# Performance work log

Measured on AMD Instinct MI355X. Metric: run time of the kernel, lower is better.

## Reference

```python
import jax, jax.numpy as jnp
import numpy as np

B, T, D, H, KH = 4, 2048, 2048, 32, 64  # batch, seq, n_dim(=n_dim_att), heads, head_size
DMIX, DDEC, NMIX = 32, 64, 5
N_LAYER, LAYER_ID = 24, 0


def setup_inputs() -> dict:
    key = jax.random.key(0)
    ks = jax.random.split(key, 16)
    rn = lambda k, s, scale: jax.random.normal(k, s, jnp.float32) * scale
    un = lambda k, s: jax.random.uniform(k, s, jnp.float32, -0.01, 0.01)

    # init-formula parameters (layer_id=0 -> ratio_0_to_1=0, ratio_1_to_almost0=1)
    ddd = np.arange(D, dtype=np.float32) / D
    tmx = (1.0 - ddd)[None, None, :]
    tmr = (1.0 - ddd ** 0.5)[None, None, :]
    n = np.arange(D, dtype=np.float32)
    decay_speed = (-6.0 + 5.0 * (n / (D - 1)) ** 0.7)[None, None, :]

    inp = {
        'x': rn(ks[0], (B, T, D), 1.0),
        'shift_state_in': rn(ks[1], (B, D), 1.0),
        'wkv_state_in': rn(ks[2], (B, H, KH, KH), 0.1),
        'time_maa_x': jnp.asarray(tmx),
        'time_maa_r': jnp.asarray(tmr),
        'time_maa_k': jnp.asarray(tmx),
        'time_maa_v': jnp.asarray(tmx),
        'time_maa_w': jnp.asarray(tmx),
        'time_maa_v2': jnp.asarray(tmx),
        'time_maa_w1': un(ks[3], (D, NMIX * DMIX)),
        'time_maa_w2': un(ks[4], (NMIX, DMIX, D)),
        'time_decay': jnp.asarray(decay_speed),
        'time_decay_w1': un(ks[5], (D, DDEC)),
        'time_decay_w2': un(ks[6], (DDEC, D)),
        'time_value2_w1': un(ks[7], (D, DDEC)),
        'time_value2_w2': un(ks[8], (DDEC, D)),
        'W_r': rn(ks[9], (D, D), 0.02),
        'W_k': rn(ks[10], (D, D), 0.02),
        'W_v': rn(ks[11], (D, D), 0.02),
        'W_o': rn(ks[12], (D, D), 0.02),
        'ln_w': jnp.ones((D,), jnp.float32),
        'ln_b': jnp.zeros((D,), jnp.float32),
    }
    return inp


def reference(x, shift_state_in, wkv_state_in,
              time_maa_x, time_maa_r, time_maa_k, time_maa_v, time_maa_w, time_maa_v2,
              time_maa_w1, time_maa_w2, time_decay, time_decay_w1, time_decay_w2,
              time_value2_w1, time_value2_w2, W_r, W_k, W_v, W_o, ln_w, ln_b):
    b, t, d = x.shape
    h, kh = wkv_state_in.shape[1], wkv_state_in.shape[2]

    shift_state_out = x[:, -1]
    xprev = jnp.concatenate([shift_state_in[:, None, :], x[:, :-1]], axis=1)
    dxprev = xprev - x  # [b,t,d]

    # low-rank token-shift mixing: tanh(x @ w1) -> 5 mixing deltas
    xxx = x + dxprev * time_maa_x
    mix = jnp.tanh(xxx @ time_maa_w1).reshape(b, t, NMIX, -1)
    mix = jnp.einsum('btfm,fmd->fbtd', mix, time_maa_w2)  # [5,b,t,d]
    mr, mk, mv, mw, mv2 = mix[0], mix[1], mix[2], mix[3], mix[4]

    xr = x + dxprev * (time_maa_r + mr)
    xk = x + dxprev * (time_maa_k + mk)
    xv = x + dxprev * (time_maa_v + mv)
    xw = x + dxprev * (time_maa_w + mw)
    xv2 = x + dxprev * (time_maa_v2 + mv2)

    r = xr @ W_r
    k = xk @ W_k
    v = xv @ W_v
    # note: v2 uses the SAME value projection plus a low-rank tanh branch
    v2 = xv2 @ W_v + jnp.tanh(xv2 @ time_value2_w1) @ time_value2_w2

    w = time_decay + jnp.tanh(xw @ time_decay_w1) @ time_decay_w2
    decay = jnp.exp(-jnp.exp(w))  # per-channel decay in (0,1)
    k = k * (1.0 - decay)

    # WKV linear-attention recurrence (u = 0): y_t = r_t . S_{t-1};  S_t = decay_t*S_{t-1} + k_t v_t^T
    to_heads = lambda a: a.reshape(b, t, h, kh).transpose(1, 0, 2, 3)  # [t,b,h,kh]
    rt, kt, vt, dt = to_heads(r), to_heads(k), to_heads(v), to_heads(decay)

    def step(S, inp):
        r_, k_, v_, d_ = inp  # each [b,h,kh]
        y = jnp.einsum('bhk,bhkv->bhv', r_, S)
        S = S * d_[..., None] + k_[..., None] * v_[:, :, None, :]
        return S, y

    wkv_state_out, ys = jax.lax.scan(step, wkv_state_in, (rt, kt, vt, dt))
    y = ys.transpose(1, 0, 2, 3).reshape(b, t, d) + v2

    # LayerNorm (ln_x)
    mu = y.mean(-1, keepdims=True)
    var = ((y - mu) ** 2).mean(-1, keepdims=True)
    y = (y - mu) / jnp.sqrt(var + 1e-5) * ln_w + ln_b

    out = y @ W_o
    return out, shift_state_out, wkv_state_out
```

## Files before the change

kernel.cpp:

```cpp
#include <hip/hip_runtime.h>
#include <hip/hip_bf16.h>

typedef __attribute__((ext_vector_type(8))) short   vshort8;
typedef __attribute__((ext_vector_type(8))) unsigned short vushort8;
typedef __attribute__((ext_vector_type(4))) float   vfloat4;
typedef __attribute__((ext_vector_type(2))) float   vfloat2;

__device__ __forceinline__ float bf2f(unsigned short h) {
    union { unsigned u; float f; } x; x.u = ((unsigned)h) << 16; return x.f;
}
__device__ __forceinline__ unsigned short f2bf(float f) {
    union { float f; unsigned u; } x; x.f = f;
    unsigned r = x.u + 0x7fffu + ((x.u >> 16) & 1u);
    return (unsigned short)(r >> 16);
}
__device__ __forceinline__ void cp16_async(const void* g, void* l) {
    __builtin_amdgcn_global_load_lds(
        (const __attribute__((address_space(1))) unsigned int*)g,
        (__attribute__((address_space(3))) unsigned int*)l, 16, 0, 0);
}

#define FBAR() do { asm volatile("" ::: "memory"); __builtin_amdgcn_s_barrier(); asm volatile("" ::: "memory"); } while (0)

#define Bc 4
#define Tc 2048
#define Dc 2048
#define Hc 32
#define KHc 64
#define BTc (Bc*Tc)
#define BTDc ((size_t)BTc*Dc)
#define LP 72

struct EpiP {
    float* of;
    unsigned short* ob;
    const float* a0;
    const float* a1;
    const unsigned short* ab;
    const float* vec;
};

template<int EPI>
__device__ __forceinline__ void epi_store(float a, int row, int col, int N, const EpiP& ep)
{
    size_t o = (size_t)row * N + col;
    if (EPI == 0) {
        ep.of[o] = a;
    } else if (EPI == 1) {
        ep.ob[o] = f2bf(a);
    } else if (EPI == 2) {
        ep.ob[o] = f2bf(tanhf(a));
    } else if (EPI == 4) {
        ep.ob[o] = f2bf(a * (1.f - ep.a0[o]));
    } else if (EPI == 5) {
        ep.of[o] = expf(-expf(ep.vec[col] + a));
    } else if (EPI == 6) {
        ep.ob[o] = f2bf(a + bf2f(ep.ab[o]));
    }
}

template<int EPI>
__global__ __launch_bounds__(256) void gemm_bt(
    const unsigned short* __restrict__ A, int lda,
    const unsigned short* __restrict__ BT, int ldbt,
    int M, int N, int K, EpiP ep)
{
    __shared__ unsigned short lA[128 * 32];
    __shared__ unsigned short lB[128 * 32];
    const int tid  = threadIdx.x;
    const int lane = tid & 63;
    const int w    = tid >> 6;
    const int mt   = blockIdx.y, nt = blockIdx.x;
    const int wm = (w >> 1) * 64, wn = (w & 1) * 64;
    const int frow = lane & 15, fk = (lane >> 4) * 8;

    vfloat4 acc[4][4];
#pragma unroll
    for (int i = 0; i < 4; i++)
#pragma unroll
        for (int j = 0; j < 4; j++) acc[i][j] = vfloat4{0.f, 0.f, 0.f, 0.f};

    for (int k0 = 0; k0 < K; k0 += 32) {
        __syncthreads();
#pragma unroll
        for (int p = 0; p < 2; p++) {
            int idx = p * 256 + tid;
            int row = idx >> 2, colh = (idx & 3) * 8;
            cp16_async(A + (size_t)(mt * 128 + row) * lda + k0 + colh, &lA[idx * 8]);
        }
#pragma unroll
        for (int p = 0; p < 2; p++) {
            int idx = p * 256 + tid;
            int row = idx >> 2, colh = (idx & 3) * 8;
            cp16_async(BT + (size_t)(nt * 128 + row) * ldbt + k0 + colh, &lB[idx * 8]);
        }
        __syncthreads();

        vshort8 af[4], bfr[4];
#pragma unroll
        for (int m = 0; m < 4; m++) af[m]  = *(const vshort8*)&lA[(wm + m * 16 + frow) * 32 + fk];
#pragma unroll
        for (int n = 0; n < 4; n++) bfr[n] = *(const vshort8*)&lB[(wn + n * 16 + frow) * 32 + fk];
#pragma unroll
        for (int m = 0; m < 4; m++)
#pragma unroll
            for (int n = 0; n < 4; n++)
                acc[m][n] = __builtin_amdgcn_mfma_f32_16x16x32_bf16(af[m], bfr[n], acc[m][n], 0, 0, 0);
    }

    const int crow0 = mt * 128 + wm, ccol0 = nt * 128 + wn;
#pragma unroll
    for (int m = 0; m < 4; m++)
#pragma unroll
        for (int n = 0; n < 4; n++) {
            int col = ccol0 + n * 16 + (lane & 15);
            if (col >= N) continue;
#pragma unroll
            for (int q = 0; q < 4; q++) {
                int row = crow0 + m * 16 + (lane >> 4) * 4 + q;
                epi_store<EPI>(acc[m][n][q], row, col, N, ep);
            }
        }
}

template<int EPI>
__global__ __launch_bounds__(512, 1) void gemm256s(
    const unsigned short* __restrict__ A, int lda,
    const unsigned short* __restrict__ BT, int ldbt,
    int M, int N, int K, EpiP ep)
{
    __shared__ unsigned short sh[3 * 16384];
    const int tid  = threadIdx.x;
    const int lane = tid & 63;
    const int w    = tid >> 6;

    int bid = blockIdx.y * gridDim.x + blockIdx.x;
    {
        int nwg = gridDim.x * gridDim.y;
        if ((nwg & 7) == 0) bid = (bid & 7) * (nwg >> 3) + (bid >> 3);
    }
    const int mt = bid / gridDim.x, nt = bid % gridDim.x;

    const int wm = (w >> 2) * 128, wn = (w & 3) * 64;
    const int frow = lane & 15;
    const int cswz = ((lane >> 4) ^ ((frow >> 1) & 3)) * 8;
    const int arow0 = mt * 256, brow0 = nt * 256;

    vfloat4 acc[8][4];
#pragma unroll
    for (int i = 0; i < 8; i++)
#pragma unroll
        for (int j = 0; j < 4; j++) acc[i][j] = vfloat4{0.f, 0.f, 0.f, 0.f};

    const int NT = K >> 5;

    auto stage = [&](int kt, int sbuf) {
        int k0 = kt << 5;
        unsigned short* dst = &sh[sbuf * 16384];
#pragma unroll
        for (int i = 0; i < 2; i++) {
            int idx = i * 512 + tid;
            int row = idx >> 2;
            int ch  = (idx & 3) ^ ((row >> 1) & 3);
            cp16_async(A + (size_t)(arow0 + row) * lda + k0 + ch * 8, dst + idx * 8);
        }
#pragma unroll
        for (int i = 0; i < 2; i++) {
            int idx = i * 512 + tid;
            int row = idx >> 2;
            int ch  = (idx & 3) ^ ((row >> 1) & 3);
            cp16_async(BT + (size_t)(brow0 + row) * ldbt + k0 + ch * 8, dst + 8192 + idx * 8);
        }
    };

    stage(0, 0);
    if (NT > 1) {
        stage(1, 1);
        asm volatile("s_waitcnt vmcnt(4)" ::: "memory");
    } else {
        asm volatile("s_waitcnt vmcnt(0)" ::: "memory");
    }
    __builtin_amdgcn_s_barrier();

    int buf = 0, sb = 2;
    for (int kt = 0; kt < NT; kt++) {
        if (kt + 2 < NT) stage(kt + 2, sb);
        const unsigned short* Ab = &sh[buf * 16384];
        const unsigned short* Bb = Ab + 8192;

        vshort8 af[8], bfv[4];
#pragma unroll
        for (int m = 0; m < 8; m++)
            af[m] = *(const vshort8*)&Ab[(wm + m * 16 + frow) * 32 + cswz];
#pragma unroll
        for (int n = 0; n < 4; n++)
            bfv[n] = *(const vshort8*)&Bb[(wn + n * 16 + frow) * 32 + cswz];

        __builtin_amdgcn_s_setprio(1);
#pragma unroll
        for (int m = 0; m < 8; m++)
#pragma unroll
            for (int n = 0; n < 4; n++)
                acc[m][n] = __builtin_amdgcn_mfma_f32_16x16x32_bf16(af[m], bfv[n], acc[m][n], 0, 0, 0);
        __builtin_amdgcn_s_setprio(0);

        if (kt + 1 < NT) {
            if (kt + 2 < NT) asm volatile("s_waitcnt vmcnt(4)" ::: "memory");
            else             asm volatile("s_waitcnt vmcnt(0)" ::: "memory");
            asm volatile("s_waitcnt lgkmcnt(0)" ::: "memory");
            __builtin_amdgcn_s_barrier();
        }
        buf = (buf == 2) ? 0 : buf + 1;
        sb  = (sb  == 2) ? 0 : sb  + 1;
    }

    const int crow0 = arow0 + wm, ccol0 = brow0 + wn;
#pragma unroll
    for (int m = 0; m < 8; m++)
#pragma unroll
        for (int n = 0; n < 4; n++) {
            int col = ccol0 + n * 16 + (lane & 15);
#pragma unroll
            for (int q = 0; q < 4; q++) {
                int row = crow0 + m * 16 + (lane >> 4) * 4 + q;
                epi_store<EPI>(acc[m][n][q], row, col, N, ep);
            }
        }
}

template<int EPI>
__global__ __launch_bounds__(512, 1) void gemm256p8(
    const unsigned short* __restrict__ A, int lda,
    const unsigned short* __restrict__ BT, int ldbt,
    int M, int N, int K, EpiP ep)
{
    __shared__ unsigned short sh[65536];
    const int tid  = threadIdx.x;
    const int lane = tid & 63;
    const int w    = tid >> 6;

    int bid = blockIdx.y * gridDim.x + blockIdx.x;
    {
        int nwg = gridDim.x * gridDim.y;
        if ((nwg & 7) == 0) bid = (bid & 7) * (nwg >> 3) + (bid >> 3);
    }
    const int mt = bid / gridDim.x, nt = bid % gridDim.x;

    const int wm = (w >> 2) * 128, wn = (w & 3) * 64;
    const int frow = lane & 15;
    const int g    = lane >> 4;
    const int arow0 = mt * 256, brow0 = nt * 256;

    vfloat4 acc[8][4];
#pragma unroll
    for (int i = 0; i < 8; i++)
#pragma unroll
        for (int j = 0; j < 4; j++) acc[i][j] = vfloat4{0.f, 0.f, 0.f, 0.f};

    const int NT = K >> 6;

    auto stageA = [&](int kt, int p) {
        int k0 = kt << 6;
        unsigned short* dst = &sh[(kt & 1) * 32768];
#pragma unroll
        for (int l = 0; l < 2; l++) {
            int idx  = l * 512 + tid;
            int rl   = idx >> 3, slot = idx & 7;
            int rg   = (rl & 63) + p * 64 + ((rl >> 6) << 7);
            int ch   = slot ^ (rg & 7);
            cp16_async(A + (size_t)(arow0 + rg) * lda + k0 + ch * 8, dst + rg * 64 + slot * 8);
        }
    };
    auto stageB = [&](int kt, int p) {
        int k0 = kt << 6;
        unsigned short* dst = &sh[(kt & 1) * 32768 + 16384];
#pragma unroll
        for (int l = 0; l < 2; l++) {
            int idx  = l * 512 + tid;
            int rl   = idx >> 3, slot = idx & 7;
            int rg   = (rl & 31) + p * 32 + ((rl >> 5) << 6);
            int ch   = slot ^ (rg & 7);
            cp16_async(BT + (size_t)(brow0 + rg) * ldbt + k0 + ch * 8, dst + rg * 64 + slot * 8);
        }
    };

    vshort8 af[4][2], bf0[2][2], bf1[2][2];

    auto readA = [&](const unsigned short* Ab, int mh) {
#pragma unroll
        for (int mi = 0; mi < 4; mi++) {
            int r = wm + mh * 64 + mi * 16 + frow;
#pragma unroll
            for (int kk = 0; kk < 2; kk++)
                af[mi][kk] = *(const vshort8*)&Ab[r * 64 + (((kk * 4 + g) ^ (r & 7)) * 8)];
        }
    };
    auto readB = [&](const unsigned short* Bb, int nh, vshort8 (&bfr)[2][2]) {
#pragma unroll
        for (int ni = 0; ni < 2; ni++) {
            int r = wn + nh * 32 + ni * 16 + frow;
#pragma unroll
            for (int kk = 0; kk < 2; kk++)
                bfr[ni][kk] = *(const vshort8*)&Bb[r * 64 + (((kk * 4 + g) ^ (r & 7)) * 8)];
        }
    };
    auto domfma = [&](int mh, int nh, vshort8 (&bfr)[2][2]) {
        __builtin_amdgcn_s_setprio(1);
#pragma unroll
        for (int mi = 0; mi < 4; mi++)
#pragma unroll
            for (int ni = 0; ni < 2; ni++)
#pragma unroll
                for (int kk = 0; kk < 2; kk++)
                    acc[mh * 4 + mi][nh * 2 + ni] = __builtin_amdgcn_mfma_f32_16x16x32_bf16(
                        af[mi][kk], bfr[ni][kk], acc[mh * 4 + mi][nh * 2 + ni], 0, 0, 0);
        __builtin_amdgcn_s_setprio(0);
    };

    stageA(0, 0); stageB(0, 1); stageA(0, 1); stageB(0, 0);
    stageA(1, 0); stageB(1, 1);
    asm volatile("s_waitcnt vmcnt(4)" ::: "memory");
    __builtin_amdgcn_s_barrier();

    const unsigned short* A0 = sh;
    const unsigned short* B0 = sh + 16384;
    const unsigned short* A1 = sh + 32768;
    const unsigned short* B1 = sh + 49152;

    for (int i2 = 0; i2 < NT; i2 += 2) {
        const bool s2 = (i2 + 2 < NT);
        readA(A0, 0); readB(B0, 0, bf0);
        stageA(i2 + 1, 1);
        FBAR();
        asm volatile("s_waitcnt lgkmcnt(0)" ::: "memory");
        domfma(0, 0, bf0);
        FBAR();
        readB(B0, 1, bf1);
        stageB(i2 + 1, 0);
        FBAR();
        asm volatile("s_waitcnt lgkmcnt(0)" ::: "memory");
        domfma(0, 1, bf1);
        FBAR();
        readA(A0, 1);
        if (s2) stageA(i2 + 2, 0);
        FBAR();
        asm volatile("s_waitcnt lgkmcnt(0)" ::: "memory");
        domfma(1, 1, bf1);
        FBAR();
        if (s2) {
            stageB(i2 + 2, 1);
            asm volatile("s_waitcnt vmcnt(4)" ::: "memory");
        } else {
            asm volatile("s_waitcnt vmcnt(0)" ::: "memory");
        }
        FBAR();
        domfma(1, 0, bf0);
        FBAR();
        readA(A1, 0); readB(B1, 0, bf0);
        if (s2) stageA(i2 + 2, 1);
        FBAR();
        asm volatile("s_waitcnt lgkmcnt(0)" ::: "memory");
        domfma(0, 0, bf0);
        FBAR();
        readB(B1, 1, bf1);
        if (s2) stageB(i2 + 2, 0);
        FBAR();
        asm volatile("s_waitcnt lgkmcnt(0)" ::: "memory");
        domfma(0, 1, bf1);
        FBAR();
        readA(A1, 1);
        if (s2) stageA(i2 + 3, 0);
        FBAR();
        asm volatile("s_waitcnt lgkmcnt(0)" ::: "memory");
        domfma(1, 1, bf1);
        FBAR();
        if (s2) {
            stageB(i2 + 3, 1);
            asm volatile("s_waitcnt vmcnt(4)" ::: "memory");
        }
        FBAR();
        domfma(1, 0, bf0);
        FBAR();
    }

    const int crow0 = arow0 + wm, ccol0 = brow0 + wn;
#pragma unroll
    for (int m = 0; m < 8; m++)
#pragma unroll
        for (int n = 0; n < 4; n++) {
            int col = ccol0 + n * 16 + (lane & 15);
#pragma unroll
            for (int q = 0; q < 4; q++) {
                int row = crow0 + m * 16 + (lane >> 4) * 4 + q;
                epi_store<EPI>(acc[m][n][q], row, col, N, ep);
            }
        }
}

struct Mix5P {
    const float* vec[5];
    unsigned short* out[5];
};

__global__ __launch_bounds__(256) void mix5(
    const unsigned short* __restrict__ MP,
    const unsigned short* __restrict__ W2T,
    const float* __restrict__ x,
    const unsigned short* __restrict__ DXb,
    Mix5P p)
{
    __shared__ unsigned short lA[64 * 32];
    __shared__ unsigned short lB[128 * 32];
    const int tid = threadIdx.x, lane = tid & 63, w = tid >> 6;
    const int mt = blockIdx.y, nt = blockIdx.x;
    const int wm = (w >> 1) * 32, wn = (w & 1) * 64;
    const int frow = lane & 15, fk = (lane >> 4) * 8;
    const int row0 = mt * 64, col0 = nt * 128;

    float xr[8][4], dxr[8][4];
#pragma unroll
    for (int mi = 0; mi < 2; mi++)
#pragma unroll
        for (int q = 0; q < 4; q++) {
            int rl = wm + mi * 16 + (lane >> 4) * 4 + q;
            size_t rb = (size_t)(row0 + rl) * Dc + col0;
#pragma unroll
            for (int ni = 0; ni < 4; ni++) {
                int cl = wn + ni * 16 + (lane & 15);
                xr[mi * 4 + q][ni]  = x[rb + cl];
                dxr[mi * 4 + q][ni] = bf2f(DXb[rb + cl]);
            }
        }

    for (int f = 0; f < 5; f++) {
        __syncthreads();
        {
            int row = tid >> 2, ch = tid & 3;
            cp16_async(MP + (size_t)(row0 + row) * 160 + f * 32 + ch * 8, &lA[(row * 4 + ch) * 8]);
        }
#pragma unroll
        for (int p2 = 0; p2 < 2; p2++) {
            int idx = p2 * 256 + tid;
            int row = idx >> 2, ch = idx & 3;
            cp16_async(W2T + (size_t)(col0 + row) * 160 + f * 32 + ch * 8, &lB[(row * 4 + ch) * 8]);
        }
        __syncthreads();

        vshort8 af[2], bfr[4];
#pragma unroll
        for (int mi = 0; mi < 2; mi++) af[mi]  = *(const vshort8*)&lA[(wm + mi * 16 + frow) * 32 + fk];
#pragma unroll
        for (int ni = 0; ni < 4; ni++) bfr[ni] = *(const vshort8*)&lB[(wn + ni * 16 + frow) * 32 + fk];

        vfloat4 acc[2][4];
#pragma unroll
        for (int mi = 0; mi < 2; mi++)
#pragma unroll
            for (int ni = 0; ni < 4; ni++) {
                acc[mi][ni] = vfloat4{0.f, 0.f, 0.f, 0.f};
                acc[mi][ni] = __builtin_amdgcn_mfma_f32_16x16x32_bf16(af[mi], bfr[ni], acc[mi][ni], 0, 0, 0);
            }

        const float* vec = p.vec[f];
        unsigned short* ob = p.out[f];
        float vc[4];
#pragma unroll
        for (int ni = 0; ni < 4; ni++) vc[ni] = vec[col0 + wn + ni * 16 + (lane & 15)];
#pragma unroll
        for (int mi = 0; mi < 2; mi++)
#pragma unroll
            for (int q = 0; q < 4; q++) {
                int rl = wm + mi * 16 + (lane >> 4) * 4 + q;
                size_t rb = (size_t)(row0 + rl) * Dc + col0;
#pragma unroll
                for (int ni = 0; ni < 4; ni++) {
                    int cl = wn + ni * 16 + (lane & 15);
                    ob[rb + cl] = f2bf(xr[mi * 4 + q][ni] + dxr[mi * 4 + q][ni] * (vc[ni] + acc[mi][ni][q]));
                }
            }
    }
}

__global__ __launch_bounds__(256) void prep_xxx(
    const float* __restrict__ x, const float* __restrict__ shift_in,
    const float* __restrict__ tmx, unsigned short* __restrict__ xxx,
    unsigned short* __restrict__ dxb)
{
    int row = blockIdx.x, tid = threadIdx.x;
    int t = row & (Tc - 1), b = row >> 11;
    size_t base = (size_t)row * Dc + tid * 8;
    const float* xp = t ? x + base - Dc : shift_in + (size_t)b * Dc + tid * 8;
    vushort8 o, dxo;
#pragma unroll
    for (int j = 0; j < 8; j++) {
        float xv = x[base + j];
        float dx = xp[j] - xv;
        o[j]   = f2bf(xv + dx * tmx[tid * 8 + j]);
        dxo[j] = f2bf(dx);
    }
    *(vushort8*)(xxx + base) = o;
    *(vushort8*)(dxb + base) = dxo;
}

__global__ __launch_bounds__(256) void shift_copy(const float* __restrict__ x, float* __restrict__ out)
{
    int i = blockIdx.x * 256 + threadIdx.x;
    int b = i >> 11, d = i & (Dc - 1);
    out[i] = x[((size_t)b * Tc + (Tc - 1)) * Dc + d];
}

__global__ __launch_bounds__(256) void transpose_cast(
    const float* __restrict__ in, unsigned short* __restrict__ out, int R, int C)
{
    __shared__ float tile[32][33];
    int ct = blockIdx.x, rt = blockIdx.y;
    int lx = threadIdx.x & 31, ly = threadIdx.x >> 5;
#pragma unroll
    for (int i = 0; i < 4; i++)
        tile[ly + i * 8][lx] = in[(size_t)(rt * 32 + ly + i * 8) * C + ct * 32 + lx];
    __syncthreads();
#pragma unroll
    for (int i = 0; i < 4; i++)
        out[(size_t)(ct * 32 + ly + i * 8) * R + rt * 32 + lx] = f2bf(tile[lx][ly + i * 8]);
}

__global__ __launch_bounds__(256) void wkv_summary(
    const unsigned short* __restrict__ kd, const unsigned short* __restrict__ vv,
    const float* __restrict__ dec, float* __restrict__ P, float* __restrict__ aL)
{
    __shared__ unsigned short kb2T[64][LP];
    __shared__ unsigned short vT[64][LP];
    __shared__ float gp[4][64];
    const int blk = blockIdx.x;
    const int c = blk & 31, bh = blk >> 5, b = bh >> 5, h = bh & 31;
    const int tid = threadIdx.x;
    const size_t rowbase = ((size_t)(b * Tc + c * 64)) * Dc + h * 64;

    {
        int t = tid >> 2, q = tid & 3;
        const unsigned short* src = vv + rowbase + (size_t)t * Dc + q * 16;
        vushort8 a = *(const vushort8*)src;
        vushort8 b2 = *(const vushort8*)(src + 8);
#pragma unroll
        for (int j = 0; j < 8; j++) vT[q * 16 + j][t] = a[j];
#pragma unroll
        for (int j = 0; j < 8; j++) vT[q * 16 + 8 + j][t] = b2[j];
    }

    const int k = tid & 63, grp = tid >> 6;
    const float* decp = dec + rowbase + k;
    const unsigned short* kp = kd + rowbase + k;
    float suf_local[16];
    float pgrp = 1.f;
#pragma unroll
    for (int i = 15; i >= 0; i--) {
        int t = grp * 16 + i;
        float d = decp[(size_t)t * Dc];
        suf_local[i] = pgrp;
        pgrp *= d;
    }
    gp[grp][k] = pgrp;
    __syncthreads();
    float suff = 1.f;
#pragma unroll
    for (int g2 = 0; g2 < 4; g2++) if (g2 > grp) suff *= gp[g2][k];
    if (grp == 0) aL[(size_t)blk * 64 + k] = pgrp * suff;
    {
        vushort8 p0, p1;
#pragma unroll
        for (int i = 0; i < 8; i++) {
            int t = grp * 16 + i;
            p0[i] = f2bf(bf2f(kp[(size_t)t * Dc]) * (suf_local[i] * suff));
        }
#pragma unroll
        for (int i = 0; i < 8; i++) {
            int t = grp * 16 + 8 + i;
            p1[i] = f2bf(bf2f(kp[(size_t)t * Dc]) * (suf_local[8 + i] * suff));
        }
        *(vushort8*)&kb2T[k][grp * 16] = p0;
        *(vushort8*)&kb2T[k][grp * 16 + 8] = p1;
    }
    __syncthreads();

    const int lane = tid & 63, w = tid >> 6;
    const int wm = (w >> 1) * 32, wn = (w & 1) * 32;
    const int frow = lane & 15, fk = (lane >> 4) * 8;
    vfloat4 acc[2][2];
#pragma unroll
    for (int m = 0; m < 2; m++)
#pragma unroll
        for (int n = 0; n < 2; n++) acc[m][n] = vfloat4{0.f, 0.f, 0.f, 0.f};
#pragma unroll
    for (int kk = 0; kk < 2; kk++) {
        vshort8 af[2], bfr[2];
#pragma unroll
        for (int m = 0; m < 2; m++) af[m]  = *(const vshort8*)&kb2T[wm + m * 16 + frow][kk * 32 + fk];
#pragma unroll
        for (int n = 0; n < 2; n++) bfr[n] = *(const vshort8*)&vT[wn + n * 16 + frow][kk * 32 + fk];
#pragma unroll
        for (int m = 0; m < 2; m++)
#pragma unroll
            for (int n = 0; n < 2; n++)
                acc[m][n] = __builtin_amdgcn_mfma_f32_16x16x32_bf16(af[m], bfr[n], acc[m][n], 0, 0, 0);
    }
    float* Pp = P + (size_t)blk * 4096;
#pragma unroll
    for (int m = 0; m < 2; m++)
#pragma unroll
        for (int n = 0; n < 2; n++) {
            int col = wn + n * 16 + (lane & 15);
#pragma unroll
            for (int q = 0; q < 4; q++) {
                int row = wm + m * 16 + (lane >> 4) * 4 + q;
                Pp[row * 64 + col] = acc[m][n][q];
            }
        }
}

__global__ __launch_bounds__(256) void wkv_states(
    const float* __restrict__ wkv_in, float* __restrict__ P ,
    const float* __restrict__ aL, float* __restrict__ wkv_out)
{
    int idx = blockIdx.x * 256 + threadIdx.x;
    int bh = idx >> 12, kv = idx & 4095, k = kv >> 6;
    float S = wkv_in[idx];
    for (int c = 0; c < 32; c++) {
        size_t off = (size_t)bh * 32 + c;
        float p = P[off * 4096 + kv];
        float a = aL[off * 64 + k];
        P[off * 4096 + kv] = S;
        S = S * a + p;
    }
    wkv_out[idx] = S;
}

__global__ __launch_bounds__(256) void wkv_y(
    const unsigned short* __restrict__ rr, const unsigned short* __restrict__ kd,
    const unsigned short* __restrict__ vv, const float* __restrict__ dec,
    const float* __restrict__ Sb, unsigned short* __restrict__ ya)
{
    __shared__ unsigned short rA[64][LP];
    __shared__ unsigned short kbL[64][LP];
    __shared__ unsigned short vT[64][LP];
    __shared__ unsigned short SbT[64][LP];
    __shared__ unsigned short QiM[64][LP];
    __shared__ float gp[4][64];
    const int blk = blockIdx.x;
    const int c = blk & 31, bh = blk >> 5, b = bh >> 5, h = bh & 31;
    const int tid = threadIdx.x;
    const size_t rowbase = ((size_t)(b * Tc + c * 64)) * Dc + h * 64;

    {
        int t = tid >> 2, q = tid & 3;
        const unsigned short* src = vv + rowbase + (size_t)t * Dc + q * 16;
        vushort8 a = *(const vushort8*)src;
        vushort8 b2 = *(const vushort8*)(src + 8);
#pragma unroll
        for (int j = 0; j < 8; j++) vT[q * 16 + j][t] = a[j];
#pragma unroll
        for (int j = 0; j < 8; j++) vT[q * 16 + 8 + j][t] = b2[j];
        const float* sp = Sb + (size_t)blk * 4096 + t * 64 + q * 16;
#pragma unroll
        for (int j = 0; j < 16; j++) SbT[q * 16 + j][t] = f2bf(sp[j]);
    }

    const int k = tid & 63, grp = tid >> 6;
    const float* decp = dec + rowbase + k;
    const unsigned short* rp = rr + rowbase + k;
    const unsigned short* kp = kd + rowbase + k;
    float pref_local[16];
    float pgrp = 1.f;
#pragma unroll
    for (int i = 0; i < 16; i++) {
        int t = grp * 16 + i;
        float d = decp[(size_t)t * Dc];
        pref_local[i] = pgrp;
        pgrp *= d;
    }
    gp[grp][k] = pgrp;
    __syncthreads();
    float pref = 1.f;
#pragma unroll
    for (int g2 = 0; g2 < 4; g2++) if (g2 < grp) pref *= gp[g2][k];
#pragma unroll
    for (int i = 0; i < 16; i++) {
        int t = grp * 16 + i;
        float Aex  = pref * pref_local[i];
        float Ainc = pref * (i < 15 ? pref_local[i + 1] : pgrp);
        rA[t][k]  = f2bf(bf2f(rp[(size_t)t * Dc]) * Aex);
        kbL[t][k] = f2bf(bf2f(kp[(size_t)t * Dc]) / Ainc);
    }
    __syncthreads();

    const int lane = tid & 63, w = tid >> 6;
    const int wm = (w >> 1) * 32, wn = (w & 1) * 32;
    const int frow = lane & 15, fk = (lane >> 4) * 8;

    vfloat4 acc[2][2];
#pragma unroll
    for (int m = 0; m < 2; m++)
#pragma unroll
        for (int n = 0; n < 2; n++) acc[m][n] = vfloat4{0.f, 0.f, 0.f, 0.f};
#pragma unroll
    for (int kk = 0; kk < 2; kk++) {
        vshort8 af[2], bfr[2];
#pragma unroll
        for (int m = 0; m < 2; m++) af[m]  = *(const vshort8*)&rA[wm + m * 16 + frow][kk * 32 + fk];
#pragma unroll
        for (int n = 0; n < 2; n++) bfr[n] = *(const vshort8*)&kbL[wn + n * 16 + frow][kk * 32 + fk];
#pragma unroll
        for (int m = 0; m < 2; m++)
#pragma unroll
            for (int n = 0; n < 2; n++)
                acc[m][n] = __builtin_amdgcn_mfma_f32_16x16x32_bf16(af[m], bfr[n], acc[m][n], 0, 0, 0);
    }
#pragma unroll
    for (int m = 0; m < 2; m++)
#pragma unroll
        for (int n = 0; n < 2; n++) {
            int s = wn + n * 16 + (lane & 15);
#pragma unroll
            for (int q = 0; q < 4; q++) {
                int t = wm + m * 16 + (lane >> 4) * 4 + q;
                QiM[t][s] = f2bf(s < t ? acc[m][n][q] : 0.f);
            }
        }
    __syncthreads();

#pragma unroll
    for (int m = 0; m < 2; m++)
#pragma unroll
        for (int n = 0; n < 2; n++) acc[m][n] = vfloat4{0.f, 0.f, 0.f, 0.f};
#pragma unroll
    for (int kk = 0; kk < 2; kk++) {
        vshort8 af[2], bfr[2];
#pragma unroll
        for (int m = 0; m < 2; m++) af[m]  = *(const vshort8*)&QiM[wm + m * 16 + frow][kk * 32 + fk];
#pragma unroll
        for (int n = 0; n < 2; n++) bfr[n] = *(const vshort8*)&vT[wn + n * 16 + frow][kk * 32 + fk];
#pragma unroll
        for (int m = 0; m < 2; m++)
#pragma unroll
            for (int n = 0; n < 2; n++)
                acc[m][n] = __builtin_amdgcn_mfma_f32_16x16x32_bf16(af[m], bfr[n], acc[m][n], 0, 0, 0);
    }
#pragma unroll
    for (int kk = 0; kk < 2; kk++) {
        vshort8 af[2], bfr[2];
#pragma unroll
        for (int m = 0; m < 2; m++) af[m]  = *(const vshort8*)&rA[wm + m * 16 + frow][kk * 32 + fk];
#pragma unroll
        for (int n = 0; n < 2; n++) bfr[n] = *(const vshort8*)&SbT[wn + n * 16 + frow][kk * 32 + fk];
#pragma unroll
        for (int m = 0; m < 2; m++)
#pragma unroll
            for (int n = 0; n < 2; n++)
                acc[m][n] = __builtin_amdgcn_mfma_f32_16x16x32_bf16(af[m], bfr[n], acc[m][n], 0, 0, 0);
    }
#pragma unroll
    for (int m = 0; m < 2; m++)
#pragma unroll
        for (int n = 0; n < 2; n++) {
            int col = wn + n * 16 + (lane & 15);
#pragma unroll
            for (int q = 0; q < 4; q++) {
                int t = wm + m * 16 + (lane >> 4) * 4 + q;
                ya[rowbase + (size_t)t * Dc + col] = f2bf(acc[m][n][q]);
            }
        }
}

__global__ __launch_bounds__(256) void ln_fuse(
    const unsigned short* __restrict__ ya, const unsigned short* __restrict__ v2,
    const float* __restrict__ lnw, const float* __restrict__ lnb,
    unsigned short* __restrict__ out)
{
    int row = blockIdx.x, tid = threadIdx.x;
    size_t base = (size_t)row * Dc + tid * 8;
    vushort8 a = *(const vushort8*)(ya + base);
    vushort8 b = *(const vushort8*)(v2 + base);
    float v[8]; float s = 0.f, s2 = 0.f;
#pragma unroll
    for (int j = 0; j < 8; j++) { float t = bf2f(a[j]) + bf2f(b[j]); v[j] = t; s += t; s2 += t * t; }
#pragma unroll
    for (int o = 32; o; o >>= 1) { s += __shfl_xor(s, o); s2 += __shfl_xor(s2, o); }
    __shared__ float rs[8];
    int w = tid >> 6;
    if ((tid & 63) == 0) { rs[w] = s; rs[w + 4] = s2; }
    __syncthreads();
    s  = rs[0] + rs[1] + rs[2] + rs[3];
    s2 = rs[4] + rs[5] + rs[6] + rs[7];
    float mu = s * (1.f / Dc);
    float var = s2 * (1.f / Dc) - mu * mu;
    float inv = rsqrtf(var + 1e-5f);
#pragma unroll
    for (int j = 0; j < 8; j++) {
        int d = tid * 8 + j;
        out[base + j] = f2bf((v[j] - mu) * inv * lnw[d] + lnb[d]);
    }
}

static inline void launch_gemm(int epi, const unsigned short* A, int lda,
                               const unsigned short* BT, int ldbt,
                               int M, int N, int K, EpiP ep, hipStream_t s)
{
    if ((M & 255) == 0 && (N & 255) == 0) {
        if ((K & 127) == 0 && K >= 128 && (epi == 0 || epi == 1 || epi == 4)) {
            dim3 g(N / 256, M / 256), b(512);
            switch (epi) {
                case 0: gemm256p8<0><<<g, b, 0, s>>>(A, lda, BT, ldbt, M, N, K, ep); break;
                case 1: gemm256p8<1><<<g, b, 0, s>>>(A, lda, BT, ldbt, M, N, K, ep); break;
                case 4: gemm256p8<4><<<g, b, 0, s>>>(A, lda, BT, ldbt, M, N, K, ep); break;
            }
            return;
        }
        if ((K & 31) == 0) {
            dim3 g(N / 256, M / 256), b(512);
            switch (epi) {
                case 0: gemm256s<0><<<g, b, 0, s>>>(A, lda, BT, ldbt, M, N, K, ep); break;
                case 1: gemm256s<1><<<g, b, 0, s>>>(A, lda, BT, ldbt, M, N, K, ep); break;
                case 2: gemm256s<2><<<g, b, 0, s>>>(A, lda, BT, ldbt, M, N, K, ep); break;
                case 4: gemm256s<4><<<g, b, 0, s>>>(A, lda, BT, ldbt, M, N, K, ep); break;
                case 5: gemm256s<5><<<g, b, 0, s>>>(A, lda, BT, ldbt, M, N, K, ep); break;
                case 6: gemm256s<6><<<g, b, 0, s>>>(A, lda, BT, ldbt, M, N, K, ep); break;
            }
            return;
        }
    }
    dim3 g((N + 127) / 128, M / 128), b(256);
    switch (epi) {
        case 0: gemm_bt<0><<<g, b, 0, s>>>(A, lda, BT, ldbt, M, N, K, ep); break;
        case 1: gemm_bt<1><<<g, b, 0, s>>>(A, lda, BT, ldbt, M, N, K, ep); break;
        case 2: gemm_bt<2><<<g, b, 0, s>>>(A, lda, BT, ldbt, M, N, K, ep); break;
        case 4: gemm_bt<4><<<g, b, 0, s>>>(A, lda, BT, ldbt, M, N, K, ep); break;
        case 5: gemm_bt<5><<<g, b, 0, s>>>(A, lda, BT, ldbt, M, N, K, ep); break;
        case 6: gemm_bt<6><<<g, b, 0, s>>>(A, lda, BT, ldbt, M, N, K, ep); break;
    }
}

extern "C" void kernel_launch(void* const* d_in, const int* in_sizes, int n_in,
                              void* d_out, int out_size, void* d_ws, size_t ws_size,
                              hipStream_t stream)
{
    (void)in_sizes; (void)n_in; (void)out_size; (void)ws_size;
    const float* x      = (const float*)d_in[0];
    const float* shift  = (const float*)d_in[1];
    const float* wkv_in = (const float*)d_in[2];
    const float* tmx    = (const float*)d_in[3];
    const float* tmr    = (const float*)d_in[4];
    const float* tmk    = (const float*)d_in[5];
    const float* tmv    = (const float*)d_in[6];
    const float* tmw    = (const float*)d_in[7];
    const float* tmv2   = (const float*)d_in[8];
    const float* w1     = (const float*)d_in[9];
    const float* w2     = (const float*)d_in[10];
    const float* tdecay = (const float*)d_in[11];
    const float* tdw1   = (const float*)d_in[12];
    const float* tdw2   = (const float*)d_in[13];
    const float* tv2w1  = (const float*)d_in[14];
    const float* tv2w2  = (const float*)d_in[15];
    const float* Wr     = (const float*)d_in[16];
    const float* Wk     = (const float*)d_in[17];
    const float* Wv     = (const float*)d_in[18];
    const float* Wo     = (const float*)d_in[19];
    const float* lnw    = (const float*)d_in[20];
    const float* lnb    = (const float*)d_in[21];

    char* ws = (char*)d_ws;
    const size_t BF = 2 * BTDc;
    size_t o = 0;
    auto take = [&](size_t bytes) { size_t r = o; o += (bytes + 255) & ~(size_t)255; return r; };
    unsigned short* WrT    = (unsigned short*)(ws + take((size_t)Dc * Dc * 2));
    unsigned short* WkT    = (unsigned short*)(ws + take((size_t)Dc * Dc * 2));
    unsigned short* WvT    = (unsigned short*)(ws + take((size_t)Dc * Dc * 2));
    unsigned short* WoT    = (unsigned short*)(ws + take((size_t)Dc * Dc * 2));
    unsigned short* w1T    = (unsigned short*)(ws + take((size_t)160 * Dc * 2));
    unsigned short* w2T    = (unsigned short*)(ws + take((size_t)Dc * 160 * 2));
    unsigned short* tdw1T  = (unsigned short*)(ws + take((size_t)64 * Dc * 2));
    unsigned short* tdw2T  = (unsigned short*)(ws + take((size_t)Dc * 64 * 2));
    unsigned short* tv2w1T = (unsigned short*)(ws + take((size_t)64 * Dc * 2));
    unsigned short* tv2w2T = (unsigned short*)(ws + take((size_t)Dc * 64 * 2));
    take(1 << 18);
    unsigned short* S0     = (unsigned short*)(ws + take(BF));
    unsigned short* MIXPRE = (unsigned short*)(ws + take((size_t)BTc * 160 * 2));
    unsigned short* S1     = (unsigned short*)(ws + take(BF));
    unsigned short* WT     = (unsigned short*)(ws + take((size_t)BTc * 64 * 2));
    unsigned short* T1     = (unsigned short*)(ws + take((size_t)BTc * 64 * 2));
    unsigned short* S2     = (unsigned short*)(ws + take(BF));
    unsigned short* S3     = (unsigned short*)(ws + take(BF));
    unsigned short* S4     = (unsigned short*)(ws + take(BF));
    float*          Pb     = (float*)(ws + take((size_t)128 * 32 * 4096 * 4));
    float*          ALb    = (float*)(ws + take((size_t)128 * 32 * 64 * 4));

    float* out_f     = (float*)d_out;
    float* shift_out = out_f + BTDc;
    float* wkv_out   = shift_out + (size_t)Bc * Dc;
    float* DEC       = out_f;

    unsigned short* XXX = S0;
    unsigned short* DX  = S4;
    unsigned short* XR  = S0;
    unsigned short* XK  = S1;
    unsigned short* XV  = S2;
    unsigned short* XW  = S3;
    unsigned short* XV2 = S4;
    unsigned short* KDb = S3;
    unsigned short* Vb  = S1;
    unsigned short* Rb  = S2;
    unsigned short* YA  = S0;
    unsigned short* V2  = S3;
    unsigned short* YLN = S1;

    dim3 tb(256);
    transpose_cast<<<dim3(64, 64), tb, 0, stream>>>(Wr, WrT, Dc, Dc);
    transpose_cast<<<dim3(64, 64), tb, 0, stream>>>(Wk, WkT, Dc, Dc);
    transpose_cast<<<dim3(64, 64), tb, 0, stream>>>(Wv, WvT, Dc, Dc);
    transpose_cast<<<dim3(64, 64), tb, 0, stream>>>(Wo, WoT, Dc, Dc);
    transpose_cast<<<dim3(5, 64),  tb, 0, stream>>>(w1, w1T, Dc, 160);
    transpose_cast<<<dim3(64, 5),  tb, 0, stream>>>(w2, w2T, 160, Dc);
    transpose_cast<<<dim3(2, 64),  tb, 0, stream>>>(tdw1, tdw1T, Dc, 64);
    transpose_cast<<<dim3(64, 2),  tb, 0, stream>>>(tdw2, tdw2T, 64, Dc);
    transpose_cast<<<dim3(2, 64),  tb, 0, stream>>>(tv2w1, tv2w1T, Dc, 64);
    transpose_cast<<<dim3(64, 2),  tb, 0, stream>>>(tv2w2, tv2w2T, 64, Dc);

    prep_xxx<<<BTc, tb, 0, stream>>>(x, shift, tmx, XXX, DX);
    shift_copy<<<32, tb, 0, stream>>>(x, shift_out);

    EpiP ep{};
    ep = EpiP{}; ep.ob = MIXPRE;
    launch_gemm(2, XXX, Dc, w1T, Dc, BTc, 160, Dc, ep, stream);

    {
        Mix5P mp;
        mp.vec[0] = tmr; mp.vec[1] = tmk; mp.vec[2] = tmv; mp.vec[3] = tmw; mp.vec[4] = tmv2;
        mp.out[0] = XR;  mp.out[1] = XK;  mp.out[2] = XV;  mp.out[3] = XW;  mp.out[4] = XV2;
        mix5<<<dim3(16, 128), tb, 0, stream>>>(MIXPRE, w2T, x, DX, mp);
    }

    ep = EpiP{}; ep.ob = WT;
    launch_gemm(2, XW, Dc, tdw1T, Dc, BTc, 64, Dc, ep, stream);
    ep = EpiP{}; ep.of = DEC; ep.vec = tdecay;
    launch_gemm(5, WT, 64, tdw2T, 64, BTc, Dc, 64, ep, stream);
    ep = EpiP{}; ep.ob = KDb; ep.a0 = DEC;
    launch_gemm(4, XK, Dc, WkT, Dc, BTc, Dc, Dc, ep, stream);
    ep = EpiP{}; ep.ob = Vb;
    launch_gemm(1, XV, Dc, WvT, Dc, BTc, Dc, Dc, ep, stream);
    ep = EpiP{}; ep.ob = Rb;
    launch_gemm(1, XR, Dc, WrT, Dc, BTc, Dc, Dc, ep, stream);

    wkv_summary<<<4096, tb, 0, stream>>>(KDb, Vb, DEC, Pb, ALb);
    wkv_states<<<2048, tb, 0, stream>>>(wkv_in, Pb, ALb, wkv_out);
    wkv_y<<<4096, tb, 0, stream>>>(Rb, KDb, Vb, DEC, Pb, YA);

    ep = EpiP{}; ep.ob = V2;
    launch_gemm(1, XV2, Dc, WvT, Dc, BTc, Dc, Dc, ep, stream);
    ep = EpiP{}; ep.ob = T1;
    launch_gemm(2, XV2, Dc, tv2w1T, Dc, BTc, 64, Dc, ep, stream);
    ep = EpiP{}; ep.ob = V2; ep.ab = V2;
    launch_gemm(6, T1, 64, tv2w2T, 64, BTc, Dc, 64, ep, stream);

    ln_fuse<<<BTc, tb, 0, stream>>>(YA, V2, lnw, lnb, YLN);
    ep = EpiP{}; ep.of = out_f;
    launch_gemm(0, YLN, Dc, WoT, Dc, BTc, Dc, Dc, ep, stream);
}
```

Measured before the change: 828.4 us.

## Replace 256x256 ping-pong GEMM with 128x128 three-stage tile kernel

Removes the eight-phase ping-pong 256x256 GEMM and routes all GEMMs with 128-aligned shapes to a new 128x128 tile kernel with 256 threads and a three-buffer cp.async-style pipeline. The intent is higher workgroup counts, more resident waves per CU and simpler synchronisation with fewer barriers. The trade-off is lower data reuse per tile, so global and LDS traffic per MFMA doubles, and the carefully interleaved load/compute schedule is lost.

```diff
diff --git a/kernel.cpp b/kernel.cpp
--- a/kernel.cpp
+++ b/kernel.cpp
@@ -19,8 +19,6 @@
         (const __attribute__((address_space(1))) unsigned int*)g,
         (__attribute__((address_space(3))) unsigned int*)l, 16, 0, 0);
 }
-
-#define FBAR() do { asm volatile("" ::: "memory"); __builtin_amdgcn_s_barrier(); asm volatile("" ::: "memory"); } while (0)
 
 #define Bc 4
 #define Tc 2048
@@ -124,12 +122,12 @@
 }
 
 template<int EPI>
-__global__ __launch_bounds__(512, 1) void gemm256s(
+__global__ __launch_bounds__(256) void gemm128t(
     const unsigned short* __restrict__ A, int lda,
     const unsigned short* __restrict__ BT, int ldbt,
     int M, int N, int K, EpiP ep)
 {
-    __shared__ unsigned short sh[3 * 16384];
+    __shared__ unsigned short sh[3 * 8192];
     const int tid  = threadIdx.x;
     const int lane = tid & 63;
     const int w    = tid >> 6;
@@ -141,14 +139,14 @@
     }
     const int mt = bid / gridDim.x, nt = bid % gridDim.x;
 
-    const int wm = (w >> 2) * 128, wn = (w & 3) * 64;
+    const int wm = (w >> 1) * 64, wn = (w & 1) * 64;
     const int frow = lane & 15;
     const int cswz = ((lane >> 4) ^ ((frow >> 1) & 3)) * 8;
-    const int arow0 = mt * 256, brow0 = nt * 256;
-
-    vfloat4 acc[8][4];
-#pragma unroll
-    for (int i = 0; i < 8; i++)
+    const int arow0 = mt * 128, brow0 = nt * 128;
+
+    vfloat4 acc[4][4];
+#pragma unroll
+    for (int i = 0; i < 4; i++)
 #pragma unroll
         for (int j = 0; j < 4; j++) acc[i][j] = vfloat4{0.f, 0.f, 0.f, 0.f};
 
@@ -156,20 +154,20 @@
 
     auto stage = [&](int kt, int sbuf) {
         int k0 = kt << 5;
-        unsigned short* dst = &sh[sbuf * 16384];
+        unsigned short* dst = &sh[sbuf * 8192];
 #pragma unroll
         for (int i = 0; i < 2; i++) {
-            int idx = i * 512 + tid;
+            int idx = i * 256 + tid;
             int row = idx >> 2;
             int ch  = (idx & 3) ^ ((row >> 1) & 3);
             cp16_async(A + (size_t)(arow0 + row) * lda + k0 + ch * 8, dst + idx * 8);
         }
 #pragma unroll
         for (int i = 0; i < 2; i++) {
-            int idx = i * 512 + tid;
+            int idx = i * 256 + tid;
             int row = idx >> 2;
             int ch  = (idx & 3) ^ ((row >> 1) & 3);
-            cp16_async(BT + (size_t)(brow0 + row) * ldbt + k0 + ch * 8, dst + 8192 + idx * 8);
+            cp16_async(BT + (size_t)(brow0 + row) * ldbt + k0 + ch * 8, dst + 4096 + idx * 8);
         }
     };
 
@@ -185,23 +183,23 @@
     int buf = 0, sb = 2;
     for (int kt = 0; kt < NT; kt++) {
         if (kt + 2 < NT) stage(kt + 2, sb);
-        const unsigned short* Ab = &sh[buf * 16384];
-        const unsigned short* Bb = Ab + 8192;
-
-        vshort8 af[8], bfv[4];
-#pragma unroll
-        for (int m = 0; m < 8; m++)
+        const unsigned short* Ab = &sh[buf * 8192];
+        const unsigned short* Bb = Ab + 4096;
+
+        vshort8 af[4], bfr[4];
+#pragma unroll
+        for (int m = 0; m < 4; m++)
             af[m] = *(const vshort8*)&Ab[(wm + m * 16 + frow) * 32 + cswz];
 #pragma unroll
         for (int n = 0; n < 4; n++)
-            bfv[n] = *(const vshort8*)&Bb[(wn + n * 16 + frow) * 32 + cswz];
+            bfr[n] = *(const vshort8*)&Bb[(wn + n * 16 + frow) * 32 + cswz];
 
         __builtin_amdgcn_s_setprio(1);
 #pragma unroll
-        for (int m = 0; m < 8; m++)
+        for (int m = 0; m < 4; m++)
 #pragma unroll
             for (int n = 0; n < 4; n++)
-                acc[m][n] = __builtin_amdgcn_mfma_f32_16x16x32_bf16(af[m], bfv[n], acc[m][n], 0, 0, 0);
+                acc[m][n] = __builtin_amdgcn_mfma_f32_16x16x32_bf16(af[m], bfr[n], acc[m][n], 0, 0, 0);
         __builtin_amdgcn_s_setprio(0);
 
         if (kt + 1 < NT) {
@@ -216,7 +214,7 @@
 
     const int crow0 = arow0 + wm, ccol0 = brow0 + wn;
 #pragma unroll
-    for (int m = 0; m < 8; m++)
+    for (int m = 0; m < 4; m++)
 #pragma unroll
         for (int n = 0; n < 4; n++) {
             int col = ccol0 + n * 16 + (lane & 15);
@@ -229,12 +227,12 @@
 }
 
 template<int EPI>
-__global__ __launch_bounds__(512, 1) void gemm256p8(
+__global__ __launch_bounds__(512, 1) void gemm256s(
     const unsigned short* __restrict__ A, int lda,
     const unsigned short* __restrict__ BT, int ldbt,
     int M, int N, int K, EpiP ep)
 {
-    __shared__ unsigned short sh[65536];
+    __shared__ unsigned short sh[3 * 16384];
     const int tid  = threadIdx.x;
     const int lane = tid & 63;
     const int w    = tid >> 6;
@@ -248,7 +246,7 @@
 
     const int wm = (w >> 2) * 128, wn = (w & 3) * 64;
     const int frow = lane & 15;
-    const int g    = lane >> 4;
+    const int cswz = ((lane >> 4) ^ ((frow >> 1) & 3)) * 8;
     const int arow0 = mt * 256, brow0 = nt * 256;
 
     vfloat4 acc[8][4];
@@ -257,130 +255,66 @@
 #pragma unroll
         for (int j = 0; j < 4; j++) acc[i][j] = vfloat4{0.f, 0.f, 0.f, 0.f};
 
-    const int NT = K >> 6;
-
-    auto stageA = [&](int kt, int p) {
-        int k0 = kt << 6;
-        unsigned short* dst = &sh[(kt & 1) * 32768];
-#pragma unroll
-        for (int l = 0; l < 2; l++) {
-            int idx  = l * 512 + tid;
-            int rl   = idx >> 3, slot = idx & 7;
-            int rg   = (rl & 63) + p * 64 + ((rl >> 6) << 7);
-            int ch   = slot ^ (rg & 7);
-            cp16_async(A + (size_t)(arow0 + rg) * lda + k0 + ch * 8, dst + rg * 64 + slot * 8);
+    const int NT = K >> 5;
+
+    auto stage = [&](int kt, int sbuf) {
+        int k0 = kt << 5;
+        unsigned short* dst = &sh[sbuf * 16384];
+#pragma unroll
+        for (int i = 0; i < 2; i++) {
+            int idx = i * 512 + tid;
+            int row = idx >> 2;
+            int ch  = (idx & 3) ^ ((row >> 1) & 3);
+            cp16_async(A + (size_t)(arow0 + row) * lda + k0 + ch * 8, dst + idx * 8);
+        }
+#pragma unroll
+        for (int i = 0; i < 2; i++) {
+            int idx = i * 512 + tid;
+            int row = idx >> 2;
+            int ch  = (idx & 3) ^ ((row >> 1) & 3);
+            cp16_async(BT + (size_t)(brow0 + row) * ldbt + k0 + ch * 8, dst + 8192 + idx * 8);
         }
     };
-    auto stageB = [&](int kt, int p) {
-        int k0 = kt << 6;
-        unsigned short* dst = &sh[(kt & 1) * 32768 + 16384];
-#pragma unroll
-        for (int l = 0; l < 2; l++) {
-            int idx  = l * 512 + tid;
-            int rl   = idx >> 3, slot = idx & 7;
-            int rg   = (rl & 31) + p * 32 + ((rl >> 5) << 6);
-            int ch   = slot ^ (rg & 7);
-            cp16_async(BT + (size_t)(brow0 + rg) * ldbt + k0 + ch * 8, dst + rg * 64 + slot * 8);
-        }
-    };
-
-    vshort8 af[4][2], bf0[2][2], bf1[2][2];
-
-    auto readA = [&](const unsigned short* Ab, int mh) {
-#pragma unroll
-        for (int mi = 0; mi < 4; mi++) {
-            int r = wm + mh * 64 + mi * 16 + frow;
-#pragma unroll
-            for (int kk = 0; kk < 2; kk++)
-                af[mi][kk] = *(const vshort8*)&Ab[r * 64 + (((kk * 4 + g) ^ (r & 7)) * 8)];
-        }
-    };
-    auto readB = [&](const unsigned short* Bb, int nh, vshort8 (&bfr)[2][2]) {
-#pragma unroll
-        for (int ni = 0; ni < 2; ni++) {
-            int r = wn + nh * 32 + ni * 16 + frow;
-#pragma unroll
-            for (int kk = 0; kk < 2; kk++)
-                bfr[ni][kk] = *(const vshort8*)&Bb[r * 64 + (((kk * 4 + g) ^ (r & 7)) * 8)];
-        }
-    };
-    auto domfma = [&](int mh, int nh, vshort8 (&bfr)[2][2]) {
+
+    stage(0, 0);
+    if (NT > 1) {
+        stage(1, 1);
+        asm volatile("s_waitcnt vmcnt(4)" ::: "memory");
+    } else {
+        asm volatile("s_waitcnt vmcnt(0)" ::: "memory");
+    }
+    __builtin_amdgcn_s_barrier();
+
+    int buf = 0, sb = 2;
+    for (int kt = 0; kt < NT; kt++) {
+        if (kt + 2 < NT) stage(kt + 2, sb);
+        const unsigned short* Ab = &sh[buf * 16384];
+        const unsigned short* Bb = Ab + 8192;
+
+        vshort8 af[8], bfv[4];
+#pragma unroll
+        for (int m = 0; m < 8; m++)
+            af[m] = *(const vshort8*)&Ab[(wm + m * 16 + frow) * 32 + cswz];
+#pragma unroll
+        for (int n = 0; n < 4; n++)
+            bfv[n] = *(const vshort8*)&Bb[(wn + n * 16 + frow) * 32 + cswz];
+
         __builtin_amdgcn_s_setprio(1);
 #pragma unroll
-        for (int mi = 0; mi < 4; mi++)
-#pragma unroll
-            for (int ni = 0; ni < 2; ni++)
-#pragma unroll
-                for (int kk = 0; kk < 2; kk++)
-                    acc[mh * 4 + mi][nh * 2 + ni] = __builtin_amdgcn_mfma_f32_16x16x32_bf16(
-                        af[mi][kk], bfr[ni][kk], acc[mh * 4 + mi][nh * 2 + ni], 0, 0, 0);
+        for (int m = 0; m < 8; m++)
+#pragma unroll
+            for (int n = 0; n < 4; n++)
+                acc[m][n] = __builtin_amdgcn_mfma_f32_16x16x32_bf16(af[m], bfv[n], acc[m][n], 0, 0, 0);
         __builtin_amdgcn_s_setprio(0);
-    };
-
-    stageA(0, 0); stageB(0, 1); stageA(0, 1); stageB(0, 0);
-    stageA(1, 0); stageB(1, 1);
-    asm volatile("s_waitcnt vmcnt(4)" ::: "memory");
-    __builtin_amdgcn_s_barrier();
-
-    const unsigned short* A0 = sh;
-    const unsigned short* B0 = sh + 16384;
-    const unsigned short* A1 = sh + 32768;
-    const unsigned short* B1 = sh + 49152;
-
-    for (int i2 = 0; i2 < NT; i2 += 2) {
-        const bool s2 = (i2 + 2 < NT);
-        readA(A0, 0); readB(B0, 0, bf0);
-        stageA(i2 + 1, 1);
-        FBAR();
-        asm volatile("s_waitcnt lgkmcnt(0)" ::: "memory");
-        domfma(0, 0, bf0);
-        FBAR();
-        readB(B0, 1, bf1);
-        stageB(i2 + 1, 0);
-        FBAR();
-        asm volatile("s_waitcnt lgkmcnt(0)" ::: "memory");
-        domfma(0, 1, bf1);
-        FBAR();
-        readA(A0, 1);
-        if (s2) stageA(i2 + 2, 0);
-        FBAR();
-        asm volatile("s_waitcnt lgkmcnt(0)" ::: "memory");
-        domfma(1, 1, bf1);
-        FBAR();
-        if (s2) {
-            stageB(i2 + 2, 1);
-            asm volatile("s_waitcnt vmcnt(4)" ::: "memory");
-        } else {
-            asm volatile("s_waitcnt vmcnt(0)" ::: "memory");
-        }
-        FBAR();
-        domfma(1, 0, bf0);
-        FBAR();
-        readA(A1, 0); readB(B1, 0, bf0);
-        if (s2) stageA(i2 + 2, 1);
-        FBAR();
-        asm volatile("s_waitcnt lgkmcnt(0)" ::: "memory");
-        domfma(0, 0, bf0);
-        FBAR();
-        readB(B1, 1, bf1);
-        if (s2) stageB(i2 + 2, 0);
-        FBAR();
-        asm volatile("s_waitcnt lgkmcnt(0)" ::: "memory");
-        domfma(0, 1, bf1);
-        FBAR();
-        readA(A1, 1);
-        if (s2) stageA(i2 + 3, 0);
-        FBAR();
-        asm volatile("s_waitcnt lgkmcnt(0)" ::: "memory");
-        domfma(1, 1, bf1);
-        FBAR();
-        if (s2) {
-            stageB(i2 + 3, 1);
-            asm volatile("s_waitcnt vmcnt(4)" ::: "memory");
-        }
-        FBAR();
-        domfma(1, 0, bf0);
-        FBAR();
+
+        if (kt + 1 < NT) {
+            if (kt + 2 < NT) asm volatile("s_waitcnt vmcnt(4)" ::: "memory");
+            else             asm volatile("s_waitcnt vmcnt(0)" ::: "memory");
+            asm volatile("s_waitcnt lgkmcnt(0)" ::: "memory");
+            __builtin_amdgcn_s_barrier();
+        }
+        buf = (buf == 2) ? 0 : buf + 1;
+        sb  = (sb  == 2) ? 0 : sb  + 1;
     }
 
     const int crow0 = arow0 + wm, ccol0 = brow0 + wn;
@@ -804,28 +738,29 @@
                                const unsigned short* BT, int ldbt,
                                int M, int N, int K, EpiP ep, hipStream_t s)
 {
-    if ((M & 255) == 0 && (N & 255) == 0) {
-        if ((K & 127) == 0 && K >= 128 && (epi == 0 || epi == 1 || epi == 4)) {
-            dim3 g(N / 256, M / 256), b(512);
-            switch (epi) {
-                case 0: gemm256p8<0><<<g, b, 0, s>>>(A, lda, BT, ldbt, M, N, K, ep); break;
-                case 1: gemm256p8<1><<<g, b, 0, s>>>(A, lda, BT, ldbt, M, N, K, ep); break;
-                case 4: gemm256p8<4><<<g, b, 0, s>>>(A, lda, BT, ldbt, M, N, K, ep); break;
-            }
-            return;
-        }
-        if ((K & 31) == 0) {
-            dim3 g(N / 256, M / 256), b(512);
-            switch (epi) {
-                case 0: gemm256s<0><<<g, b, 0, s>>>(A, lda, BT, ldbt, M, N, K, ep); break;
-                case 1: gemm256s<1><<<g, b, 0, s>>>(A, lda, BT, ldbt, M, N, K, ep); break;
-                case 2: gemm256s<2><<<g, b, 0, s>>>(A, lda, BT, ldbt, M, N, K, ep); break;
-                case 4: gemm256s<4><<<g, b, 0, s>>>(A, lda, BT, ldbt, M, N, K, ep); break;
-                case 5: gemm256s<5><<<g, b, 0, s>>>(A, lda, BT, ldbt, M, N, K, ep); break;
-                case 6: gemm256s<6><<<g, b, 0, s>>>(A, lda, BT, ldbt, M, N, K, ep); break;
-            }
-            return;
-        }
+    if ((M & 127) == 0 && (N & 127) == 0 && (K & 31) == 0 && K >= 128) {
+        dim3 g(N / 128, M / 128), b(256);
+        switch (epi) {
+            case 0: gemm128t<0><<<g, b, 0, s>>>(A, lda, BT, ldbt, M, N, K, ep); break;
+            case 1: gemm128t<1><<<g, b, 0, s>>>(A, lda, BT, ldbt, M, N, K, ep); break;
+            case 2: gemm128t<2><<<g, b, 0, s>>>(A, lda, BT, ldbt, M, N, K, ep); break;
+            case 4: gemm128t<4><<<g, b, 0, s>>>(A, lda, BT, ldbt, M, N, K, ep); break;
+            case 5: gemm128t<5><<<g, b, 0, s>>>(A, lda, BT, ldbt, M, N, K, ep); break;
+            case 6: gemm128t<6><<<g, b, 0, s>>>(A, lda, BT, ldbt, M, N, K, ep); break;
+        }
+        return;
+    }
+    if ((M & 255) == 0 && (N & 255) == 0 && (K & 31) == 0) {
+        dim3 g(N / 256, M / 256), b(512);
+        switch (epi) {
+            case 0: gemm256s<0><<<g, b, 0, s>>>(A, lda, BT, ldbt, M, N, K, ep); break;
+            case 1: gemm256s<1><<<g, b, 0, s>>>(A, lda, BT, ldbt, M, N, K, ep); break;
+            case 2: gemm256s<2><<<g, b, 0, s>>>(A, lda, BT, ldbt, M, N, K, ep); break;
+            case 4: gemm256s<4><<<g, b, 0, s>>>(A, lda, BT, ldbt, M, N, K, ep); break;
+            case 5: gemm256s<5><<<g, b, 0, s>>>(A, lda, BT, ldbt, M, N, K, ep); break;
+            case 6: gemm256s<6><<<g, b, 0, s>>>(A, lda, BT, ldbt, M, N, K, ep); break;
+        }
+        return;
     }
     dim3 g((N + 127) / 128, M / 128), b(256);
     switch (epi) {
```

Result: slower. 915.5 us (+10.5%).
